# Kernel tuning notes

Hardware: AMD Instinct MI355X
Metric: run time of the kernel (lower is better)

Reference implementation:

```python
import jax, jax.numpy as jnp
import numpy as np

B, L, W, H = 4, 256, 256, 768
WORD_SIZE = 50000
NUM_LABELS = 10


def setup_inputs() -> dict:
    key = jax.random.key(0)
    k1, k2, k3, k4, k5, k6 = jax.random.split(key, 6)
    return {
        "word_seq": jax.random.randint(k1, (B, W), 0, WORD_SIZE),
        "hidden_state": jax.random.normal(k2, (B, L, H), dtype=jnp.float32),
        "label_value_matrix": jax.random.randint(k3, (B, L, W), 0, NUM_LABELS),
        "word_mask_metrix": jax.random.uniform(k4, (B, L, W), dtype=jnp.float32),
        "emb_a": jax.random.normal(k5, (WORD_SIZE, H), dtype=jnp.float32) * 0.02,
        "emb_c": jax.random.normal(k6, (NUM_LABELS, H), dtype=jnp.float32) * 0.02,
    }


def reference(word_seq, hidden_state, label_value_matrix, word_mask_metrix, emb_a, emb_c):
    temper = jnp.asarray(H, hidden_state.dtype) ** 0.5
    ea = emb_a[word_seq]                      # [B, W, H] gathered word keys
    u = jnp.einsum("blh,bwh->blw", hidden_state, ea) / temper
    mask = jnp.clip(word_mask_metrix, 0.0, 1.0)
    exp_u = jnp.exp(u) * mask                 # masked unnormalized attention
    p = exp_u / (jnp.sum(exp_u, axis=2, keepdims=True) + 1e-10)  # [B, L, W]
    ec = emb_c[label_value_matrix]            # [B, L, W, H] gathered label values
    o = jnp.einsum("blw,blwh->blh", p, ec)    # attention-weighted value sum
    return o + hidden_state
```

## Files before the change

kernel.cpp:

```cpp
#include <hip/hip_runtime.h>
#include <hip/hip_bf16.h>
#include <stdint.h>

#define BB 4
#define LL 256
#define WW 256
#define HH 768
#define NL 10
#define LT 16
#define WT 64
#define ASTRIDE 776

typedef __attribute__((ext_vector_type(8))) short bf16x8;
typedef __attribute__((ext_vector_type(4))) float f32x4;

__device__ inline unsigned short f2bf(float x) {
    return __builtin_bit_cast(unsigned short, __float2bfloat16(x));
}
__device__ inline bf16x8 pack8(float4 a, float4 b) {
    union { bf16x8 v; unsigned short u[8]; } r;
    r.u[0] = f2bf(a.x); r.u[1] = f2bf(a.y); r.u[2] = f2bf(a.z); r.u[3] = f2bf(a.w);
    r.u[4] = f2bf(b.x); r.u[5] = f2bf(b.y); r.u[6] = f2bf(b.z); r.u[7] = f2bf(b.w);
    return r.v;
}

__global__ __launch_bounds__(256, 1) void score_kernel(
    const int* __restrict__ word_seq,
    const float* __restrict__ hidden,
    const float* __restrict__ emb_a,
    const int* __restrict__ label,
    const float* __restrict__ mask,
    float* __restrict__ s_out)
{
    __shared__ unsigned short A_lds[LT * ASTRIDE];
    __shared__ float s_lds[LT][NL];

    const int t    = threadIdx.x;
    const int wave = t >> 6, lane = t & 63;
    const int g    = lane >> 4, c = lane & 15;

    const int x    = blockIdx.x;
    const int G    = (x & 7) + 8 * (x >> 7);
    const int lt   = (x >> 3) & 15;
    const int b    = G >> 2, wt = G & 3;
    const int l0   = lt * LT;

    if (t < LT * NL) ((float*)s_lds)[t] = 0.f;

    #pragma unroll
    for (int i = 0; i < 6; ++i) {
        int idx = t + i * 256;
        int r = idx / 96, u = idx - r * 96;
        const float4* src = reinterpret_cast<const float4*>(
            hidden + ((size_t)(b * LL) + l0 + r) * HH + u * 8);
        float4 v0 = src[0], v1 = src[1];
        *reinterpret_cast<bf16x8*>(&A_lds[r * ASTRIDE + u * 8]) = pack8(v0, v1);
    }

    const int wcol = wt * WT + wave * 16 + c;
    const int wrow = word_seq[b * WW + wcol];
    const float4* bp = reinterpret_cast<const float4*>(
        emb_a + (size_t)wrow * HH + g * 8);

    float4 rb0[4], rb1[4];
    #pragma unroll
    for (int i = 0; i < 4; ++i) { rb0[i] = bp[i * 8]; rb1[i] = bp[i * 8 + 1]; }

    __syncthreads();

    f32x4 acc = {0.f, 0.f, 0.f, 0.f};
    #pragma unroll
    for (int k = 0; k < 24; ++k) {
        const int s = k & 3;
        bf16x8 bv = pack8(rb0[s], rb1[s]);
        bf16x8 av = *reinterpret_cast<const bf16x8*>(
            &A_lds[c * ASTRIDE + (4 * k + g) * 8]);
        if (k + 4 < 24) { rb0[s] = bp[(k + 4) * 8]; rb1[s] = bp[(k + 4) * 8 + 1]; }
        acc = __builtin_amdgcn_mfma_f32_16x16x32_bf16(av, bv, acc, 0, 0, 0);
    }

    const float scale = 0.03608439182435161f;
    #pragma unroll
    for (int r = 0; r < 4; ++r) {
        int lrow = g * 4 + r;
        size_t idx = ((size_t)(b * LL) + l0 + lrow) * WW + wcol;
        float m = mask[idx];
        m = fminf(fmaxf(m, 0.f), 1.f);
        float e = __expf(acc[r] * scale) * m;
        atomicAdd(&s_lds[lrow][label[idx]], e);
    }
    __syncthreads();

    if (t < LT * NL) {
        size_t sidx = ((size_t)((b * 16 + lt) * 4 + wt)) * (LT * NL) + t;
        s_out[sidx] = ((float*)s_lds)[t];
    }
}

__global__ __launch_bounds__(192, 4) void combine_kernel(
    const float* __restrict__ s_in,
    const float* __restrict__ hidden,
    const float* __restrict__ emb_c,
    float* __restrict__ out)
{
    __shared__ float sp[LT][NL];
    __shared__ float inv[LT];
    const int t = threadIdx.x;
    const int bid = blockIdx.x;
    const int hq = bid & 3, lt = (bid >> 2) & 15, b = bid >> 6;
    const int l0 = lt * LT;
    const int h = hq * 192 + t;

    if (t < LT * NL) {
        size_t base = ((size_t)(b * 16 + lt)) * 4 * (LT * NL);
        float v = 0.f;
        #pragma unroll
        for (int wt = 0; wt < 4; ++wt) v += s_in[base + wt * (LT * NL) + t];
        ((float*)sp)[t] = v;
    }
    __syncthreads();
    if (t < LT) {
        float d = 1e-10f;
        #pragma unroll
        for (int k = 0; k < NL; ++k) d += sp[t][k];
        inv[t] = 1.f / d;
    }
    __syncthreads();

    float ec[NL];
    #pragma unroll
    for (int k = 0; k < NL; ++k) ec[k] = emb_c[k * HH + h];
    #pragma unroll
    for (int r = 0; r < LT; ++r) {
        size_t base = ((size_t)(b * LL) + l0 + r) * HH + h;
        float acc = 0.f;
        #pragma unroll
        for (int k = 0; k < NL; ++k) acc = fmaf(sp[r][k], ec[k], acc);
        out[base] = hidden[base] + acc * inv[r];
    }
}

extern "C" void kernel_launch(void* const* d_in, const int* in_sizes, int n_in,
                              void* d_out, int out_size, void* d_ws, size_t ws_size,
                              hipStream_t stream) {
    const int*   word_seq = (const int*)d_in[0];
    const float* hidden   = (const float*)d_in[1];
    const int*   label    = (const int*)d_in[2];
    const float* mask     = (const float*)d_in[3];
    const float* emb_a    = (const float*)d_in[4];
    const float* emb_c    = (const float*)d_in[5];
    float*       out      = (float*)d_out;

    float* s_out = (float*)d_ws;

    score_kernel<<<BB * 16 * 4, 256, 0, stream>>>(
        word_seq, hidden, emb_a, label, mask, s_out);
    combine_kernel<<<BB * 16 * 4, 192, 0, stream>>>(s_out, hidden, emb_c, out);
}
```

Before: 16.93 us.

## Split score kernel K loop across two wave groups with LDS reduction

Doubles the score kernel block to 512 threads so each 16-column tile is handled by two waves that each cover half of the H reduction, then combines the partial MFMA accumulators through shared memory. The mask and label loads are issued before the main loop so their latency overlaps the gather and MFMA work. This aims to cut per-wave serial latency in a latency-bound kernel that has only 256 blocks. The cost is an extra barrier, an LDS round trip, and half the waves sitting idle during the epilogue.

New measurement: 17.21 us. About the same (+1.7%).

```diff
diff --git a/kernel.cpp b/kernel.cpp
--- a/kernel.cpp
+++ b/kernel.cpp
@@ -24,7 +24,7 @@
     return r.v;
 }
 
-__global__ __launch_bounds__(256, 1) void score_kernel(
+__global__ __launch_bounds__(512, 1) void score_kernel(
     const int* __restrict__ word_seq,
     const float* __restrict__ hidden,
     const float* __restrict__ emb_a,
@@ -33,10 +33,13 @@
     float* __restrict__ s_out)
 {
     __shared__ unsigned short A_lds[LT * ASTRIDE];
+    __shared__ float partial[4][64][4];
     __shared__ float s_lds[LT][NL];
 
     const int t    = threadIdx.x;
-    const int wave = t >> 6, lane = t & 63;
+    const int wv   = t >> 6, lane = t & 63;
+    const int ti   = wv & 3;
+    const int kb   = (wv >> 2) * 12;
     const int g    = lane >> 4, c = lane & 15;
 
     const int x    = blockIdx.x;
@@ -48,8 +51,8 @@
     if (t < LT * NL) ((float*)s_lds)[t] = 0.f;
 
     #pragma unroll
-    for (int i = 0; i < 6; ++i) {
-        int idx = t + i * 256;
+    for (int i = 0; i < 3; ++i) {
+        int idx = t + i * 512;
         int r = idx / 96, u = idx - r * 96;
         const float4* src = reinterpret_cast<const float4*>(
             hidden + ((size_t)(b * LL) + l0 + r) * HH + u * 8);
@@ -57,37 +60,60 @@
         *reinterpret_cast<bf16x8*>(&A_lds[r * ASTRIDE + u * 8]) = pack8(v0, v1);
     }
 
-    const int wcol = wt * WT + wave * 16 + c;
+    const int wcol = wt * WT + ti * 16 + c;
     const int wrow = word_seq[b * WW + wcol];
     const float4* bp = reinterpret_cast<const float4*>(
         emb_a + (size_t)wrow * HH + g * 8);
 
+    float mval[4]; int lval[4];
+    if (kb == 0) {
+        #pragma unroll
+        for (int r = 0; r < 4; ++r) {
+            size_t idx = ((size_t)(b * LL) + l0 + g * 4 + r) * WW + wcol;
+            mval[r] = mask[idx];
+            lval[r] = label[idx];
+        }
+    }
+
     float4 rb0[4], rb1[4];
     #pragma unroll
-    for (int i = 0; i < 4; ++i) { rb0[i] = bp[i * 8]; rb1[i] = bp[i * 8 + 1]; }
+    for (int i = 0; i < 4; ++i) {
+        rb0[i] = bp[(kb + i) * 8];
+        rb1[i] = bp[(kb + i) * 8 + 1];
+    }
 
     __syncthreads();
 
     f32x4 acc = {0.f, 0.f, 0.f, 0.f};
     #pragma unroll
-    for (int k = 0; k < 24; ++k) {
+    for (int k = 0; k < 12; ++k) {
         const int s = k & 3;
         bf16x8 bv = pack8(rb0[s], rb1[s]);
         bf16x8 av = *reinterpret_cast<const bf16x8*>(
-            &A_lds[c * ASTRIDE + (4 * k + g) * 8]);
-        if (k + 4 < 24) { rb0[s] = bp[(k + 4) * 8]; rb1[s] = bp[(k + 4) * 8 + 1]; }
+            &A_lds[c * ASTRIDE + (4 * (kb + k) + g) * 8]);
+        if (k + 4 < 12) {
+            rb0[s] = bp[(kb + k + 4) * 8];
+            rb1[s] = bp[(kb + k + 4) * 8 + 1];
+        }
         acc = __builtin_amdgcn_mfma_f32_16x16x32_bf16(av, bv, acc, 0, 0, 0);
     }
 
-    const float scale = 0.03608439182435161f;
-    #pragma unroll
-    for (int r = 0; r < 4; ++r) {
-        int lrow = g * 4 + r;
-        size_t idx = ((size_t)(b * LL) + l0 + lrow) * WW + wcol;
-        float m = mask[idx];
-        m = fminf(fmaxf(m, 0.f), 1.f);
-        float e = __expf(acc[r] * scale) * m;
-        atomicAdd(&s_lds[lrow][label[idx]], e);
+    if (kb != 0)
+        *reinterpret_cast<f32x4*>(&partial[ti][lane][0]) = acc;
+    __syncthreads();
+
+    if (kb == 0) {
+        f32x4 other = *reinterpret_cast<const f32x4*>(&partial[ti][lane][0]);
+        acc += other;
+
+        const float scale = 0.03608439182435161f;
+        #pragma unroll
+        for (int r = 0; r < 4; ++r) {
+            int lrow = g * 4 + r;
+            float m = fminf(fmaxf(mval[r], 0.f), 1.f);
+            float e = __expf(acc[r] * scale) * m;
+            atomicAdd(&s_lds[lrow][lval[r]], e);
+        }
     }
     __syncthreads();
 
@@ -153,7 +179,7 @@
 
     float* s_out = (float*)d_ws;
 
-    score_kernel<<<BB * 16 * 4, 256, 0, stream>>>(
+    score_kernel<<<BB * 16 * 4, 512, 0, stream>>>(
         word_seq, hidden, emb_a, label, mask, s_out);
     combine_kernel<<<BB * 16 * 4, 192, 0, stream>>>(s_out, hidden, emb_c, out);
 }
```

## Fuse score and combine kernels via last-block ticket per row group

Applied to the files above, without the earlier changes.

Merges the combine pass into the score kernel. Each block publishes its partial per-label sums, then takes a ticket on an atomic counter, and the fourth block of each row group does the normalization and output write. The residual is read back from the bf16 hidden tile already in LDS instead of re-reading fp32 hidden from global memory, and the mask and label loads are issued before the MFMA loop. This removes a kernel launch boundary and the second pass over hidden. In exchange it adds a memset launch, serializes the combine work onto one block per group, and rounds the residual term to bf16, which costs output accuracy.

Result: slower. 33.41 us (+97.4%).

```diff
diff --git a/kernel.cpp b/kernel.cpp
--- a/kernel.cpp
+++ b/kernel.cpp
@@ -17,6 +17,9 @@
 __device__ inline unsigned short f2bf(float x) {
     return __builtin_bit_cast(unsigned short, __float2bfloat16(x));
 }
+__device__ inline float bf2f(unsigned short u) {
+    return __builtin_bit_cast(float, (uint32_t)u << 16);
+}
 __device__ inline bf16x8 pack8(float4 a, float4 b) {
     union { bf16x8 v; unsigned short u[8]; } r;
     r.u[0] = f2bf(a.x); r.u[1] = f2bf(a.y); r.u[2] = f2bf(a.z); r.u[3] = f2bf(a.w);
@@ -24,16 +27,21 @@
     return r.v;
 }
 
-__global__ __launch_bounds__(256, 1) void score_kernel(
+__global__ __launch_bounds__(256, 1) void score_fused_kernel(
     const int* __restrict__ word_seq,
     const float* __restrict__ hidden,
     const float* __restrict__ emb_a,
     const int* __restrict__ label,
     const float* __restrict__ mask,
-    float* __restrict__ s_out)
+    const float* __restrict__ emb_c,
+    float* __restrict__ out,
+    float* __restrict__ s_out,
+    int* __restrict__ cnt)
 {
     __shared__ unsigned short A_lds[LT * ASTRIDE];
     __shared__ float s_lds[LT][NL];
+    __shared__ float inv[LT];
+    __shared__ int ticket;
 
     const int t    = threadIdx.x;
     const int wave = t >> 6, lane = t & 63;
@@ -62,6 +70,14 @@
     const float4* bp = reinterpret_cast<const float4*>(
         emb_a + (size_t)wrow * HH + g * 8);
 
+    float mval[4]; int lval[4];
+    #pragma unroll
+    for (int r = 0; r < 4; ++r) {
+        size_t idx = ((size_t)(b * LL) + l0 + g * 4 + r) * WW + wcol;
+        mval[r] = mask[idx];
+        lval[r] = label[idx];
+    }
+
     float4 rb0[4], rb1[4];
     #pragma unroll
     for (int i = 0; i < 4; ++i) { rb0[i] = bp[i * 8]; rb1[i] = bp[i * 8 + 1]; }
@@ -83,60 +99,66 @@
     #pragma unroll
     for (int r = 0; r < 4; ++r) {
         int lrow = g * 4 + r;
-        size_t idx = ((size_t)(b * LL) + l0 + lrow) * WW + wcol;
-        float m = mask[idx];
-        m = fminf(fmaxf(m, 0.f), 1.f);
+        float m = fminf(fmaxf(mval[r], 0.f), 1.f);
         float e = __expf(acc[r] * scale) * m;
-        atomicAdd(&s_lds[lrow][label[idx]], e);
+        atomicAdd(&s_lds[lrow][lval[r]], e);
     }
     __syncthreads();
 
+    const int grp  = b * 16 + lt;
+    if (t < LT * NL)
+        __hip_atomic_store(&s_out[((size_t)grp * 4 + wt) * (LT * NL) + t],
+                           ((float*)s_lds)[t],
+                           __ATOMIC_RELAXED, __HIP_MEMORY_SCOPE_AGENT);
+    __syncthreads();
+
+    if (t == 0) {
+        __threadfence();
+        ticket = __hip_atomic_fetch_add(&cnt[grp], 1,
+                                        __ATOMIC_ACQ_REL, __HIP_MEMORY_SCOPE_AGENT);
+    }
+    __syncthreads();
+    if (ticket != 3) return;
+
+    __threadfence();
     if (t < LT * NL) {
-        size_t sidx = ((size_t)((b * 16 + lt) * 4 + wt)) * (LT * NL) + t;
-        s_out[sidx] = ((float*)s_lds)[t];
-    }
-}
-
-__global__ __launch_bounds__(192, 4) void combine_kernel(
-    const float* __restrict__ s_in,
-    const float* __restrict__ hidden,
-    const float* __restrict__ emb_c,
-    float* __restrict__ out)
-{
-    __shared__ float sp[LT][NL];
-    __shared__ float inv[LT];
-    const int t = threadIdx.x;
-    const int bid = blockIdx.x;
-    const int hq = bid & 3, lt = (bid >> 2) & 15, b = bid >> 6;
-    const int l0 = lt * LT;
-    const int h = hq * 192 + t;
-
-    if (t < LT * NL) {
-        size_t base = ((size_t)(b * 16 + lt)) * 4 * (LT * NL);
+        const size_t base = (size_t)grp * 4 * (LT * NL);
         float v = 0.f;
         #pragma unroll
-        for (int wt = 0; wt < 4; ++wt) v += s_in[base + wt * (LT * NL) + t];
-        ((float*)sp)[t] = v;
+        for (int w2 = 0; w2 < 4; ++w2)
+            v += __hip_atomic_load(&s_out[base + w2 * (LT * NL) + t],
+                                   __ATOMIC_RELAXED, __HIP_MEMORY_SCOPE_AGENT);
+        ((float*)s_lds)[t] = v;
     }
     __syncthreads();
     if (t < LT) {
         float d = 1e-10f;
         #pragma unroll
-        for (int k = 0; k < NL; ++k) d += sp[t][k];
+        for (int k = 0; k < NL; ++k) d += s_lds[t][k];
         inv[t] = 1.f / d;
     }
     __syncthreads();
+    if (t < LT * NL) ((float*)s_lds)[t] *= inv[t / NL];
+    __syncthreads();
 
-    float ec[NL];
-    #pragma unroll
-    for (int k = 0; k < NL; ++k) ec[k] = emb_c[k * HH + h];
-    #pragma unroll
-    for (int r = 0; r < LT; ++r) {
-        size_t base = ((size_t)(b * LL) + l0 + r) * HH + h;
-        float acc = 0.f;
+    if (t < 192) {
+        const float4* ec4 = reinterpret_cast<const float4*>(emb_c);
+        float4* o4 = reinterpret_cast<float4*>(out);
+        float4 ec[NL];
         #pragma unroll
-        for (int k = 0; k < NL; ++k) acc = fmaf(sp[r][k], ec[k], acc);
-        out[base] = hidden[base] + acc * inv[r];
+        for (int k = 0; k < NL; ++k) ec[k] = ec4[k * 192 + t];
+        #pragma unroll
+        for (int r = 0; r < LT; ++r) {
+            ushort4 hb4 = *reinterpret_cast<const ushort4*>(&A_lds[r * ASTRIDE + t * 4]);
+            float4 o = { bf2f(hb4.x), bf2f(hb4.y), bf2f(hb4.z), bf2f(hb4.w) };
+            #pragma unroll
+            for (int k = 0; k < NL; ++k) {
+                float w = s_lds[r][k];
+                o.x = fmaf(w, ec[k].x, o.x); o.y = fmaf(w, ec[k].y, o.y);
+                o.z = fmaf(w, ec[k].z, o.z); o.w = fmaf(w, ec[k].w, o.w);
+            }
+            o4[((size_t)(b * LL) + l0 + r) * 192 + t] = o;
+        }
     }
 }
 
@@ -151,9 +173,10 @@
     const float* emb_c    = (const float*)d_in[5];
     float*       out      = (float*)d_out;
 
-    float* s_out = (float*)d_ws;
+    int*   cnt   = (int*)d_ws;
+    float* s_out = (float*)((char*)d_ws + 256);
 
-    score_kernel<<<BB * 16 * 4, 256, 0, stream>>>(
-        word_seq, hidden, emb_a, label, mask, s_out);
-    combine_kernel<<<BB * 16 * 4, 192, 0, stream>>>(s_out, hidden, emb_c, out);
+    hipMemsetAsync(cnt, 0, 64 * sizeof(int), stream);
+    score_fused_kernel<<<BB * 16 * 4, 256, 0, stream>>>(
+        word_seq, hidden, emb_a, label, mask, emb_c, out, s_out, cnt);
 }
```
